# Kernel tuning notes

Hardware: AMD Instinct MI355X
Metric: run time of the kernel (lower is better)

Reference implementation:

```python
import jax, jax.numpy as jnp
import numpy as np

N_NODES = 100000
N_EDGES = 400000
N_GRAPHS = 2000
IN_DIM = 58
HEADS = 4
HID = 64           # per-head hidden = output_dim // heads = 256 // 4
OUT = 256
NEG_SLOPE = 0.2    # PyG GATConv default


def _glorot(key, shape):
    fan_in, fan_out = shape[0], shape[-1]
    lim = jnp.sqrt(6.0 / (fan_in + fan_out)).astype(jnp.float32)
    return jax.random.uniform(key, shape, jnp.float32, -lim, lim)


def setup_inputs() -> dict:
    key = jax.random.key(0)
    ks = jax.random.split(key, 16)
    x = jax.random.normal(ks[0], (N_NODES, IN_DIM), jnp.float32)
    edge_index = jax.random.randint(ks[1], (2, N_EDGES), 0, N_NODES, jnp.int64)
    batch = jnp.sort(jax.random.randint(ks[2], (N_NODES,), 0, N_GRAPHS, jnp.int64))
    return {
        "x": x,
        "edge_index": edge_index,
        "batch": batch,
        # layer 1: 58 -> 4 heads x 64, concat -> 256
        "W1": _glorot(ks[3], (IN_DIM, HEADS * HID)),
        "a_src1": _glorot(ks[4], (HEADS, HID)),
        "a_dst1": _glorot(ks[5], (HEADS, HID)),
        "b1": jnp.zeros((HEADS * HID,), jnp.float32),
        # layer 2: 256 -> 4 heads x 64, concat -> 256
        "W2": _glorot(ks[6], (HEADS * HID, HEADS * HID)),
        "a_src2": _glorot(ks[7], (HEADS, HID)),
        "a_dst2": _glorot(ks[8], (HEADS, HID)),
        "b2": jnp.zeros((HEADS * HID,), jnp.float32),
        # layer 3: 256 -> 1 head x 256, no concat (mean over 1 head)
        "W3": _glorot(ks[9], (HEADS * HID, OUT)),
        "a_src3": _glorot(ks[10], (1, OUT)),
        "a_dst3": _glorot(ks[11], (1, OUT)),
        "b3": jnp.zeros((OUT,), jnp.float32),
    }


def _gat_layer(x, src, dst, W, a_src, a_dst, b, heads, ch, concat):
    n = x.shape[0]
    h = (x @ W).reshape(n, heads, ch)                      # [N,H,C]
    e_src = jnp.einsum("nhc,hc->nh", h, a_src)             # [N,H]
    e_dst = jnp.einsum("nhc,hc->nh", h, a_dst)
    e = jax.nn.leaky_relu(e_src[src] + e_dst[dst], NEG_SLOPE)  # [E,H]
    # segment softmax over destination nodes (self-loops ensure non-empty segments)
    m = jax.ops.segment_max(e, dst, num_segments=n)
    ex = jnp.exp(e - m[dst])
    denom = jax.ops.segment_sum(ex, dst, num_segments=n)
    coef = ex / denom[dst]                                 # [E,H]
    out = jax.ops.segment_sum(h[src] * coef[:, :, None], dst, num_segments=n)
    out = out.reshape(n, heads * ch) if concat else out.mean(axis=1)
    return out + b


def reference(x, edge_index, batch, W1, a_src1, a_dst1, b1,
              W2, a_src2, a_dst2, b2, W3, a_src3, a_dst3, b3):
    n = x.shape[0]
    loops = jnp.arange(n, dtype=edge_index.dtype)
    src = jnp.concatenate([edge_index[0], loops])          # add_self_loops (PyG default)
    dst = jnp.concatenate([edge_index[1], loops])
    h = jax.nn.relu(_gat_layer(x, src, dst, W1, a_src1, a_dst1, b1, HEADS, HID, True))
    h = jax.nn.relu(_gat_layer(h, src, dst, W2, a_src2, a_dst2, b2, HEADS, HID, True))
    h = _gat_layer(h, src, dst, W3, a_src3, a_dst3, b3, 1, OUT, False)
    # global max pool over graphs
    return jax.ops.segment_max(h, batch, num_segments=N_GRAPHS)
```

## Files before the change

kernel.cpp:

```cpp
#include <hip/hip_runtime.h>
#include <hip/hip_bf16.h>
#include <math.h>

#define N_NODES_C 100000
#define E_ORIG    400000
#define E_TOT     500000
#define E_PAD     (E_TOT + 3 * N_NODES_C)
#define N_GRAPHS_C 2000
#define KDIM      256

typedef __attribute__((ext_vector_type(8))) short short8v;
typedef __attribute__((ext_vector_type(4))) float f32x4;

__device__ __forceinline__ void gload_lds16(const void* g, void* l) {
    __builtin_amdgcn_global_load_lds(
        (const __attribute__((address_space(1))) unsigned int*)g,
        (__attribute__((address_space(3))) unsigned int*)l, 16, 0, 0);
}

__device__ __forceinline__ float bflo(unsigned u) { return __uint_as_float(u << 16); }
__device__ __forceinline__ float bfhi(unsigned u) { return __uint_as_float(u & 0xffff0000u); }

#define XE  (N_NODES_C * 64)
#define W1E (256 * 64)
#define WBE (256 * 256)
__global__ __launch_bounds__(256) void conv_all_count(
        const float* __restrict__ x, const float* __restrict__ W1,
        const float* __restrict__ W2, const float* __restrict__ W3,
        const int* __restrict__ ei,
        __hip_bfloat16* __restrict__ Xb, __hip_bfloat16* __restrict__ Wt1,
        __hip_bfloat16* __restrict__ Wt2, __hip_bfloat16* __restrict__ Wt3,
        int* __restrict__ deg) {
    int idx = blockIdx.x * 256 + threadIdx.x;
    if (idx < E_TOT) {
        int d = (idx < E_ORIG) ? ei[E_ORIG + idx] : (idx - E_ORIG);
        atomicAdd(&deg[d], 1);
    }
    if (idx < XE) {
        int row = idx >> 6, c = idx & 63;
        float v = (c < 58) ? x[row * 58 + c] : 0.f;
        Xb[idx] = __float2bfloat16(v);
    } else if (idx < XE + W1E) {
        int i = idx - XE;
        int c = i >> 6, k = i & 63;
        float v = (k < 58) ? W1[k * 256 + c] : 0.f;
        Wt1[i] = __float2bfloat16(v);
    } else if (idx < XE + W1E + WBE) {
        int i = idx - XE - W1E;
        int c = i >> 8, k = i & 255;
        Wt2[i] = __float2bfloat16(W2[k * 256 + c]);
    } else if (idx < XE + W1E + 2 * WBE) {
        int i = idx - XE - W1E - WBE;
        int c = i >> 8, k = i & 255;
        Wt3[i] = __float2bfloat16(W3[k * 256 + c]);
    }
}

__global__ void scan_chunk(const int* __restrict__ in, int* __restrict__ out,
                           int* __restrict__ partials, int n) {
    __shared__ int s[256];
    int tid = threadIdx.x;
    int i = blockIdx.x * 256 + tid;
    int dv = (i < n) ? in[i] : 0;
    int v = (dv + 3) & ~3;
    s[tid] = v;
    __syncthreads();
    for (int off = 1; off < 256; off <<= 1) {
        int t = (tid >= off) ? s[tid - off] : 0;
        __syncthreads();
        s[tid] += t;
        __syncthreads();
    }
    if (i < n) out[i] = s[tid] - v;
    if (tid == 255) partials[blockIdx.x] = s[255];
}

__global__ void scan_fix(int* __restrict__ rowoff, const int* __restrict__ partials, int n) {
    __shared__ int sred[256];
    int t = threadIdx.x;
    int acc = 0;
    for (int i = t; i < blockIdx.x; i += 256) acc += partials[i];
    sred[t] = acc;
    __syncthreads();
    for (int off = 128; off; off >>= 1) {
        if (t < off) sred[t] += sred[t + off];
        __syncthreads();
    }
    int base = sred[0];
    int i = blockIdx.x * 256 + t;
    if (i < n) rowoff[i] += base;
}

__global__ void scatter_k(const int* __restrict__ ei, const int* __restrict__ rowoff,
                          int* cursor, int* __restrict__ csr_src,
                          int* __restrict__ csr_dst) {
    int e = blockIdx.x * 256 + threadIdx.x;
    if (e >= E_TOT) return;
    int s, d;
    if (e < E_ORIG) { s = ei[e]; d = ei[E_ORIG + e]; }
    else            { s = e - E_ORIG; d = s; }
    int pos = rowoff[d] + atomicAdd(&cursor[d], 1);
    csr_src[pos] = s;
    csr_dst[pos] = d;
}

__global__ void pad_fill(const int* __restrict__ deg, const int* __restrict__ rowoff,
                         int* __restrict__ csr_src, int* __restrict__ csr_dst) {
    int n = blockIdx.x * 256 + threadIdx.x;
    if (n >= N_NODES_C) return;
    int d = deg[n];
    int pd = (d + 3) & ~3;
    int base = rowoff[n];
    for (int j = d; j < pd; j++) {
        csr_src[base + j] = n | 0x80000000;
        csr_dst[base + j] = n;
    }
}

template <int KPAD, int NH>
__global__ __launch_bounds__(256, 2) void gemm_mfma(
        const __hip_bfloat16* __restrict__ Xb, const __hip_bfloat16* __restrict__ Wt,
        const float* __restrict__ ASRC, const float* __restrict__ ADST,
        __hip_bfloat16* __restrict__ H, float* __restrict__ ES, float* __restrict__ ED) {
    __shared__ char As[128 * 128];
    __shared__ char Bs[256 * 128];
    __shared__ float red[2][128][2];

    const int t = threadIdx.x;
    const int wv = t >> 6, lane = t & 63;
    const int wr = wv >> 1, wc = wv & 1;
    const int r15 = lane & 15, hi = lane >> 4;
    const int n0 = blockIdx.x * 128;
    const int srow = lane >> 3;
    const int sx = ((lane & 7) ^ srow) * 16;
    constexpr int KB = KPAD * 2;

    f32x4 acc[4][8];
#pragma unroll
    for (int m = 0; m < 4; m++)
#pragma unroll
        for (int n = 0; n < 8; n++) acc[m][n] = (f32x4){0.f, 0.f, 0.f, 0.f};

    for (int kt = 0; kt < KPAD / 64; kt++) {
        if (kt) __syncthreads();
        const int k0b = kt * 128;
#pragma unroll
        for (int p = 0; p < 4; p++) {
            int i = wv * 4 + p;
            int gr = n0 + i * 8 + srow;
            if (gr > N_NODES_C - 1) gr = N_NODES_C - 1;
            gload_lds16((const char*)Xb + (size_t)gr * KB + k0b + sx, As + i * 1024);
        }
#pragma unroll
        for (int p = 0; p < 8; p++) {
            int i = wv * 8 + p;
            int col = i * 8 + srow;
            gload_lds16((const char*)Wt + (size_t)col * KB + k0b + sx, Bs + i * 1024);
        }
        asm volatile("s_waitcnt vmcnt(0)" ::: "memory");
        __syncthreads();

#pragma unroll
        for (int ks = 0; ks < 2; ks++) {
            const int cx = ((ks * 4 + hi) ^ (r15 & 7)) * 16;
            short8v a[4];
#pragma unroll
            for (int m = 0; m < 4; m++)
                a[m] = *(const short8v*)(As + (wr * 64 + m * 16 + r15) * 128 + cx);
#pragma unroll
            for (int n = 0; n < 8; n++) {
                short8v b = *(const short8v*)(Bs + (wc * 128 + n * 16 + r15) * 128 + cx);
#pragma unroll
                for (int m = 0; m < 4; m++)
                    acc[m][n] = __builtin_amdgcn_mfma_f32_16x16x32_bf16(a[m], b, acc[m][n], 0, 0, 0);
            }
        }
    }

    float asv[8], adv[8];
#pragma unroll
    for (int n = 0; n < 8; n++) {
        int col = wc * 128 + n * 16 + r15;
        asv[n] = ASRC[col];
        adv[n] = ADST[col];
    }

#pragma unroll
    for (int m = 0; m < 4; m++) {
#pragma unroll
        for (int j = 0; j < 4; j++) {
            int lrow = wr * 64 + m * 16 + hi * 4 + j;
            int row = n0 + lrow;
            bool ok = row < N_NODES_C;
            if (ok) {
#pragma unroll
                for (int n = 0; n < 8; n++)
                    H[(size_t)row * KDIM + wc * 128 + n * 16 + r15] =
                        __float2bfloat16(acc[m][n][j]);
            }
            if (NH == 4) {
                float p0s = 0.f, p1s = 0.f, p0d = 0.f, p1d = 0.f;
#pragma unroll
                for (int n = 0; n < 4; n++) {
                    p0s = fmaf(acc[m][n][j], asv[n], p0s);
                    p0d = fmaf(acc[m][n][j], adv[n], p0d);
                    p1s = fmaf(acc[m][n + 4][j], asv[n + 4], p1s);
                    p1d = fmaf(acc[m][n + 4][j], adv[n + 4], p1d);
                }
#pragma unroll
                for (int s = 8; s; s >>= 1) {
                    p0s += __shfl_xor(p0s, s, 16);
                    p0d += __shfl_xor(p0d, s, 16);
                    p1s += __shfl_xor(p1s, s, 16);
                    p1d += __shfl_xor(p1d, s, 16);
                }
                if (r15 == 0 && ok) {
                    ES[row * 4 + wc * 2 + 0] = p0s;
                    ES[row * 4 + wc * 2 + 1] = p1s;
                    ED[row * 4 + wc * 2 + 0] = p0d;
                    ED[row * 4 + wc * 2 + 1] = p1d;
                }
            } else {
                float ps = 0.f, pd = 0.f;
#pragma unroll
                for (int n = 0; n < 8; n++) {
                    ps = fmaf(acc[m][n][j], asv[n], ps);
                    pd = fmaf(acc[m][n][j], adv[n], pd);
                }
#pragma unroll
                for (int s = 8; s; s >>= 1) {
                    ps += __shfl_xor(ps, s, 16);
                    pd += __shfl_xor(pd, s, 16);
                }
                if (r15 == 0) { red[0][lrow][wc] = ps; red[1][lrow][wc] = pd; }
            }
        }
    }
    if (NH == 1) {
        __syncthreads();
        if (t < 128) {
            int row = n0 + t;
            if (row < N_NODES_C) {
                ES[row] = red[0][t][0] + red[0][t][1];
                ED[row] = red[1][t][0] + red[1][t][1];
            }
        }
    }
}

#define ECAP 160
template <int NH, bool RELU>
__global__ __launch_bounds__(256) void agg_kernel(
        const __hip_bfloat16* __restrict__ H, const int* __restrict__ rowoff,
        const int* __restrict__ csr_src, const int* __restrict__ csr_dst,
        const float* __restrict__ ES, const float* __restrict__ ED,
        const float* __restrict__ bias, __hip_bfloat16* __restrict__ Out) {
    __shared__ float Els[ECAP * NH];
    __shared__ int   Sls[ECAP];
    __shared__ int   roff[9];
    int t = threadIdx.x;
    int n0 = blockIdx.x * 8;
    if (t < 9) roff[t] = rowoff[n0 + t];
    __syncthreads();
    int beg0 = roff[0];
    int ne = roff[8] - beg0;
    int nl = (ne < ECAP) ? ne : ECAP;
    for (int j = t; j < nl; j += 256) {
        int slot = beg0 + j;
        int srcj = csr_src[slot];
        bool padj = srcj < 0;
        srcj &= 0x7fffffff;
        int dj = csr_dst[slot];
        Sls[j] = srcj;
        if (NH == 4) {
            float4 es = *(const float4*)&ES[srcj * 4];
            float4 ed = *(const float4*)&ED[dj * 4];
            float e;
            e = es.x + ed.x; e = (e > 0.f) ? e : 0.2f * e; Els[j * 4 + 0] = padj ? -1e30f : e;
            e = es.y + ed.y; e = (e > 0.f) ? e : 0.2f * e; Els[j * 4 + 1] = padj ? -1e30f : e;
            e = es.z + ed.z; e = (e > 0.f) ? e : 0.2f * e; Els[j * 4 + 2] = padj ? -1e30f : e;
            e = es.w + ed.w; e = (e > 0.f) ? e : 0.2f * e; Els[j * 4 + 3] = padj ? -1e30f : e;
        } else {
            float e = ES[srcj] + ED[dj];
            e = (e > 0.f) ? e : 0.2f * e;
            Els[j] = padj ? -1e30f : e;
        }
    }
    __syncthreads();

    int g = t >> 5;
    int node = n0 + g;
    int l = t & 31;
    int c0 = l * 8;
    int head = (NH == 4) ? (l >> 3) : 0;
    int jb = roff[g] - beg0, je = roff[g + 1] - beg0;
    int jeF = (je < ECAP) ? je : ECAP;

    float m = -1e30f;
    for (int j = jb; j < jeF; j++) m = fmaxf(m, Els[j * NH + head]);
    if (je > ECAP) {
        float edv = ED[node * NH + head];
        for (int j = ECAP; j < je; j++) {
            int sj = csr_src[beg0 + j];
            if (sj < 0) continue;
            float e = ES[sj * NH + head] + edv;
            e = (e > 0.f) ? e : 0.2f * e;
            m = fmaxf(m, e);
        }
    }

    float s = 0.f;
    float a[8];
#pragma unroll
    for (int i = 0; i < 8; i++) a[i] = 0.f;
    const unsigned short* Hu = (const unsigned short*)H;

#define ACC8(v, p) \
    a[0] = fmaf(p, bflo(v.x), a[0]); a[1] = fmaf(p, bfhi(v.x), a[1]); \
    a[2] = fmaf(p, bflo(v.y), a[2]); a[3] = fmaf(p, bfhi(v.y), a[3]); \
    a[4] = fmaf(p, bflo(v.z), a[4]); a[5] = fmaf(p, bfhi(v.z), a[5]); \
    a[6] = fmaf(p, bflo(v.w), a[6]); a[7] = fmaf(p, bfhi(v.w), a[7]);

    int j = jb;
    for (; j + 4 <= jeF; j += 4) {
        int s0 = Sls[j], s1 = Sls[j + 1], s2 = Sls[j + 2], s3 = Sls[j + 3];
        float e0 = Els[(j + 0) * NH + head], e1 = Els[(j + 1) * NH + head];
        float e2 = Els[(j + 2) * NH + head], e3 = Els[(j + 3) * NH + head];
        uint4 v0 = *(const uint4*)(Hu + (size_t)s0 * KDIM + c0);
        uint4 v1 = *(const uint4*)(Hu + (size_t)s1 * KDIM + c0);
        uint4 v2 = *(const uint4*)(Hu + (size_t)s2 * KDIM + c0);
        uint4 v3 = *(const uint4*)(Hu + (size_t)s3 * KDIM + c0);
        float p0 = __expf(e0 - m), p1 = __expf(e1 - m);
        float p2 = __expf(e2 - m), p3 = __expf(e3 - m);
        s += p0 + p1 + p2 + p3;
        ACC8(v0, p0)
        ACC8(v1, p1)
        ACC8(v2, p2)
        ACC8(v3, p3)
    }
    for (; j < jeF; j++) {
        int s0 = Sls[j];
        float e0 = Els[j * NH + head];
        uint4 v0 = *(const uint4*)(Hu + (size_t)s0 * KDIM + c0);
        float p0 = __expf(e0 - m);
        s += p0;
        ACC8(v0, p0)
    }
    if (je > ECAP) {
        float edv = ED[node * NH + head];
        for (int jj = ECAP; jj < je; jj++) {
            int sj = csr_src[beg0 + jj];
            if (sj < 0) continue;
            float e = ES[sj * NH + head] + edv;
            e = (e > 0.f) ? e : 0.2f * e;
            float p = __expf(e - m);
            s += p;
            uint4 v = *(const uint4*)(Hu + (size_t)sj * KDIM + c0);
            ACC8(v, p)
        }
    }
#undef ACC8

    float inv = 1.f / s;
    float4 b0 = *(const float4*)&bias[c0];
    float4 b1 = *(const float4*)&bias[c0 + 4];
    float o[8];
    o[0] = fmaf(a[0], inv, b0.x); o[1] = fmaf(a[1], inv, b0.y);
    o[2] = fmaf(a[2], inv, b0.z); o[3] = fmaf(a[3], inv, b0.w);
    o[4] = fmaf(a[4], inv, b1.x); o[5] = fmaf(a[5], inv, b1.y);
    o[6] = fmaf(a[6], inv, b1.z); o[7] = fmaf(a[7], inv, b1.w);
    __hip_bfloat16 rb[8];
#pragma unroll
    for (int i = 0; i < 8; i++) {
        float v = RELU ? fmaxf(o[i], 0.f) : o[i];
        rb[i] = __float2bfloat16(v);
    }
    *(uint4*)&Out[(size_t)node * KDIM + c0] = *(uint4*)rb;
}

__global__ __launch_bounds__(256) void pool_k(
        const __hip_bfloat16* __restrict__ O, const int* __restrict__ batch,
        float* __restrict__ out) {
    __shared__ int range[2];
    __shared__ float red[3][256];
    int g = blockIdx.x, k = threadIdx.x;
    if (k < 2) {
        int v = g + k;
        int lo = 0, hi = N_NODES_C;
        while (lo < hi) { int mid = (lo + hi) >> 1; if (batch[mid] < v) lo = mid + 1; else hi = mid; }
        range[k] = lo;
    }
    __syncthreads();
    int cg = k & 63;
    int ro = k >> 6;
    float m0 = -INFINITY, m1 = -INFINITY, m2 = -INFINITY, m3 = -INFINITY;
    const unsigned short* Ou = (const unsigned short*)O;
    for (int i = range[0] + ro; i < range[1]; i += 4) {
        uint2 v = *(const uint2*)(Ou + (size_t)i * KDIM + cg * 4);
        m0 = fmaxf(m0, bflo(v.x)); m1 = fmaxf(m1, bfhi(v.x));
        m2 = fmaxf(m2, bflo(v.y)); m3 = fmaxf(m3, bfhi(v.y));
    }
    if (ro) {
        red[ro - 1][cg * 4 + 0] = m0; red[ro - 1][cg * 4 + 1] = m1;
        red[ro - 1][cg * 4 + 2] = m2; red[ro - 1][cg * 4 + 3] = m3;
    }
    __syncthreads();
    if (ro == 0) {
        m0 = fmaxf(fmaxf(m0, red[0][cg * 4 + 0]), fmaxf(red[1][cg * 4 + 0], red[2][cg * 4 + 0]));
        m1 = fmaxf(fmaxf(m1, red[0][cg * 4 + 1]), fmaxf(red[1][cg * 4 + 1], red[2][cg * 4 + 1]));
        m2 = fmaxf(fmaxf(m2, red[0][cg * 4 + 2]), fmaxf(red[1][cg * 4 + 2], red[2][cg * 4 + 2]));
        m3 = fmaxf(fmaxf(m3, red[0][cg * 4 + 3]), fmaxf(red[1][cg * 4 + 3], red[2][cg * 4 + 3]));
        float4 o = make_float4(m0, m1, m2, m3);
        *(float4*)&out[(size_t)g * KDIM + cg * 4] = o;
    }
}

extern "C" void kernel_launch(void* const* d_in, const int* in_sizes, int n_in,
                              void* d_out, int out_size, void* d_ws, size_t ws_size,
                              hipStream_t stream) {
    const float* x     = (const float*)d_in[0];
    const int*   ei    = (const int*)d_in[1];
    const int*   batch = (const int*)d_in[2];
    const float* W1  = (const float*)d_in[3];
    const float* as1 = (const float*)d_in[4];
    const float* ad1 = (const float*)d_in[5];
    const float* b1  = (const float*)d_in[6];
    const float* W2  = (const float*)d_in[7];
    const float* as2 = (const float*)d_in[8];
    const float* ad2 = (const float*)d_in[9];
    const float* b2  = (const float*)d_in[10];
    const float* W3  = (const float*)d_in[11];
    const float* as3 = (const float*)d_in[12];
    const float* ad3 = (const float*)d_in[13];
    const float* b3  = (const float*)d_in[14];
    float* out = (float*)d_out;

    char* p = (char*)d_ws;
    auto alloc = [&](size_t bytes) { char* r = p; p += (bytes + 255) & ~(size_t)255; return r; };
    __hip_bfloat16* Xb  = (__hip_bfloat16*)alloc((size_t)N_NODES_C * 64 * 2);
    __hip_bfloat16* Hb  = (__hip_bfloat16*)alloc((size_t)N_NODES_C * KDIM * 2);
    __hip_bfloat16* Nb  = (__hip_bfloat16*)alloc((size_t)N_NODES_C * KDIM * 2);
    __hip_bfloat16* Wt1 = (__hip_bfloat16*)alloc(256 * 64 * 2);
    __hip_bfloat16* Wt2 = (__hip_bfloat16*)alloc(256 * 256 * 2);
    __hip_bfloat16* Wt3 = (__hip_bfloat16*)alloc(256 * 256 * 2);
    float* ES     = (float*)alloc((size_t)N_NODES_C * 4 * 4);
    float* ED     = (float*)alloc((size_t)N_NODES_C * 4 * 4);
    int* degcur   = (int*)alloc((size_t)(2 * N_NODES_C + 1) * 4);
    int* deg      = degcur;
    int* cursor   = degcur + (N_NODES_C + 1);
    int* rowoff   = (int*)alloc((N_NODES_C + 1) * 4);
    int* csr      = (int*)alloc((size_t)E_PAD * 4 + 256);
    int* csrd     = (int*)alloc((size_t)E_PAD * 4);
    int* partials = (int*)alloc(512 * 4);

    hipMemsetAsync(degcur, 0, (size_t)(2 * N_NODES_C + 1) * 4, stream);
    int ctot = XE + W1E + 2 * WBE;
    conv_all_count<<<(ctot + 255) / 256, 256, 0, stream>>>(
        x, W1, W2, W3, ei, Xb, Wt1, Wt2, Wt3, deg);

    int nb = (N_NODES_C + 1 + 255) / 256;
    scan_chunk<<<nb, 256, 0, stream>>>(deg, rowoff, partials, N_NODES_C + 1);
    scan_fix<<<nb, 256, 0, stream>>>(rowoff, partials, N_NODES_C + 1);
    int egrid = (E_TOT + 255) / 256;
    scatter_k<<<egrid, 256, 0, stream>>>(ei, rowoff, cursor, csr, csrd);
    pad_fill<<<(N_NODES_C + 255) / 256, 256, 0, stream>>>(deg, rowoff, csr, csrd);

    int ggrid = (N_NODES_C + 127) / 128;
    int agrid = N_NODES_C / 8;
    gemm_mfma<64, 4><<<ggrid, 256, 0, stream>>>(Xb, Wt1, as1, ad1, Hb, ES, ED);
    agg_kernel<4, true><<<agrid, 256, 0, stream>>>(Hb, rowoff, csr, csrd, ES, ED, b1, Nb);
    gemm_mfma<256, 4><<<ggrid, 256, 0, stream>>>(Nb, Wt2, as2, ad2, Hb, ES, ED);
    agg_kernel<4, true><<<agrid, 256, 0, stream>>>(Hb, rowoff, csr, csrd, ES, ED, b2, Nb);
    gemm_mfma<256, 1><<<ggrid, 256, 0, stream>>>(Nb, Wt3, as3, ad3, Hb, ES, ED);
    agg_kernel<1, false><<<agrid, 256, 0, stream>>>(Hb, rowoff, csr, csrd, ES, ED, b3, Nb);
    pool_k<<<N_GRAPHS_C, 256, 0, stream>>>(Nb, batch, out);
}
```

Baseline: 319.3 us.

## Replace LDS-staged MFMA GEMM with direct global-load streaming GEMM

The GEMM kernel no longer stages X and W tiles in shared memory through global_load_lds with barriers. Each wave now loads its A rows and B columns straight from global memory into registers as it runs the MFMA loop. The block tile shrinks from 128 to 64 rows, so the grid doubles and each wave keeps half as many accumulators. This removes LDS traffic and __syncthreads stalls, but W is now reloaded per wave through cache and the global loads are less coalesced.

New measurement: 406.6 us. 27.3% more time.

```diff
diff --git a/kernel.cpp b/kernel.cpp
--- a/kernel.cpp
+++ b/kernel.cpp
@@ -11,12 +11,6 @@
 
 typedef __attribute__((ext_vector_type(8))) short short8v;
 typedef __attribute__((ext_vector_type(4))) float f32x4;
-
-__device__ __forceinline__ void gload_lds16(const void* g, void* l) {
-    __builtin_amdgcn_global_load_lds(
-        (const __attribute__((address_space(1))) unsigned int*)g,
-        (__attribute__((address_space(3))) unsigned int*)l, 16, 0, 0);
-}
 
 __device__ __forceinline__ float bflo(unsigned u) { return __uint_as_float(u << 16); }
 __device__ __forceinline__ float bfhi(unsigned u) { return __uint_as_float(u & 0xffff0000u); }
@@ -118,62 +112,41 @@
 }
 
 template <int KPAD, int NH>
-__global__ __launch_bounds__(256, 2) void gemm_mfma(
+__global__ __launch_bounds__(256, 2) void gemm_stream(
         const __hip_bfloat16* __restrict__ Xb, const __hip_bfloat16* __restrict__ Wt,
         const float* __restrict__ ASRC, const float* __restrict__ ADST,
         __hip_bfloat16* __restrict__ H, float* __restrict__ ES, float* __restrict__ ED) {
-    __shared__ char As[128 * 128];
-    __shared__ char Bs[256 * 128];
-    __shared__ float red[2][128][2];
+    __shared__ float red[2][64][2];
 
     const int t = threadIdx.x;
     const int wv = t >> 6, lane = t & 63;
     const int wr = wv >> 1, wc = wv & 1;
     const int r15 = lane & 15, hi = lane >> 4;
-    const int n0 = blockIdx.x * 128;
-    const int srow = lane >> 3;
-    const int sx = ((lane & 7) ^ srow) * 16;
+    const int n0 = blockIdx.x * 64;
     constexpr int KB = KPAD * 2;
-
-    f32x4 acc[4][8];
-#pragma unroll
-    for (int m = 0; m < 4; m++)
+    constexpr int NS = KPAD / 32;
+
+    int row0 = n0 + wr * 32 + 0 + r15;  if (row0 > N_NODES_C - 1) row0 = N_NODES_C - 1;
+    int row1 = n0 + wr * 32 + 16 + r15; if (row1 > N_NODES_C - 1) row1 = N_NODES_C - 1;
+    const char* pa0 = (const char*)Xb + (size_t)row0 * KB + hi * 16;
+    const char* pa1 = (const char*)Xb + (size_t)row1 * KB + hi * 16;
+    const char* pb  = (const char*)Wt + (size_t)(wc * 128 + r15) * KB + hi * 16;
+
+    f32x4 acc[2][8];
+#pragma unroll
+    for (int m = 0; m < 2; m++)
 #pragma unroll
         for (int n = 0; n < 8; n++) acc[m][n] = (f32x4){0.f, 0.f, 0.f, 0.f};
 
-    for (int kt = 0; kt < KPAD / 64; kt++) {
-        if (kt) __syncthreads();
-        const int k0b = kt * 128;
-#pragma unroll
-        for (int p = 0; p < 4; p++) {
-            int i = wv * 4 + p;
-            int gr = n0 + i * 8 + srow;
-            if (gr > N_NODES_C - 1) gr = N_NODES_C - 1;
-            gload_lds16((const char*)Xb + (size_t)gr * KB + k0b + sx, As + i * 1024);
-        }
-#pragma unroll
-        for (int p = 0; p < 8; p++) {
-            int i = wv * 8 + p;
-            int col = i * 8 + srow;
-            gload_lds16((const char*)Wt + (size_t)col * KB + k0b + sx, Bs + i * 1024);
-        }
-        asm volatile("s_waitcnt vmcnt(0)" ::: "memory");
-        __syncthreads();
-
-#pragma unroll
-        for (int ks = 0; ks < 2; ks++) {
-            const int cx = ((ks * 4 + hi) ^ (r15 & 7)) * 16;
-            short8v a[4];
-#pragma unroll
-            for (int m = 0; m < 4; m++)
-                a[m] = *(const short8v*)(As + (wr * 64 + m * 16 + r15) * 128 + cx);
-#pragma unroll
-            for (int n = 0; n < 8; n++) {
-                short8v b = *(const short8v*)(Bs + (wc * 128 + n * 16 + r15) * 128 + cx);
-#pragma unroll
-                for (int m = 0; m < 4; m++)
-                    acc[m][n] = __builtin_amdgcn_mfma_f32_16x16x32_bf16(a[m], b, acc[m][n], 0, 0, 0);
-            }
+#pragma unroll
+    for (int ks = 0; ks < NS; ks++) {
+        short8v a0 = *(const short8v*)(pa0 + ks * 64);
+        short8v a1 = *(const short8v*)(pa1 + ks * 64);
+#pragma unroll
+        for (int n = 0; n < 8; n++) {
+            short8v b = *(const short8v*)(pb + (size_t)n * 16 * KB + ks * 64);
+            acc[0][n] = __builtin_amdgcn_mfma_f32_16x16x32_bf16(a0, b, acc[0][n], 0, 0, 0);
+            acc[1][n] = __builtin_amdgcn_mfma_f32_16x16x32_bf16(a1, b, acc[1][n], 0, 0, 0);
         }
     }
 
@@ -186,10 +159,10 @@
     }
 
 #pragma unroll
-    for (int m = 0; m < 4; m++) {
+    for (int m = 0; m < 2; m++) {
 #pragma unroll
         for (int j = 0; j < 4; j++) {
-            int lrow = wr * 64 + m * 16 + hi * 4 + j;
+            int lrow = wr * 32 + m * 16 + hi * 4 + j;
             int row = n0 + lrow;
             bool ok = row < N_NODES_C;
             if (ok) {
@@ -238,7 +211,7 @@
     }
     if (NH == 1) {
         __syncthreads();
-        if (t < 128) {
+        if (t < 64) {
             int row = n0 + t;
             if (row < N_NODES_C) {
                 ES[row] = red[0][t][0] + red[0][t][1];
@@ -465,13 +438,13 @@
     scatter_k<<<egrid, 256, 0, stream>>>(ei, rowoff, cursor, csr, csrd);
     pad_fill<<<(N_NODES_C + 255) / 256, 256, 0, stream>>>(deg, rowoff, csr, csrd);
 
-    int ggrid = (N_NODES_C + 127) / 128;
+    int ggrid = (N_NODES_C + 63) / 64;
     int agrid = N_NODES_C / 8;
-    gemm_mfma<64, 4><<<ggrid, 256, 0, stream>>>(Xb, Wt1, as1, ad1, Hb, ES, ED);
+    gemm_stream<64, 4><<<ggrid, 256, 0, stream>>>(Xb, Wt1, as1, ad1, Hb, ES, ED);
     agg_kernel<4, true><<<agrid, 256, 0, stream>>>(Hb, rowoff, csr, csrd, ES, ED, b1, Nb);
-    gemm_mfma<256, 4><<<ggrid, 256, 0, stream>>>(Nb, Wt2, as2, ad2, Hb, ES, ED);
+    gemm_stream<256, 4><<<ggrid, 256, 0, stream>>>(Nb, Wt2, as2, ad2, Hb, ES, ED);
     agg_kernel<4, true><<<agrid, 256, 0, stream>>>(Hb, rowoff, csr, csrd, ES, ED, b2, Nb);
-    gemm_mfma<256, 1><<<ggrid, 256, 0, stream>>>(Nb, Wt3, as3, ad3, Hb, ES, ED);
+    gemm_stream<256, 1><<<ggrid, 256, 0, stream>>>(Nb, Wt3, as3, ad3, Hb, ES, ED);
     agg_kernel<1, false><<<agrid, 256, 0, stream>>>(Hb, rowoff, csr, csrd, ES, ED, b3, Nb);
     pool_k<<<N_GRAPHS_C, 256, 0, stream>>>(Nb, batch, out);
 }
```
